# Kernel optimization log

Hardware: AMD Instinct MI355X
Metric: run time of the kernel (lower is better)

The kernel has to match this reference:

```python
import jax, jax.numpy as jnp
import numpy as np

N_NODES = 100000
N_EDGES = 1600000
IN_DIM = 75
H_COMP = 64
H_BOND = 16
DEPTH = 3


def setup_inputs() -> dict:
    key = jax.random.key(0)
    ks = jax.random.split(key, 8)
    x = jax.random.normal(ks[0], (N_NODES, IN_DIM), dtype=jnp.float32)
    edge_index = jax.random.randint(ks[1], (2, N_EDGES), 0, N_NODES, dtype=jnp.int64)
    edge_attr = jax.random.normal(ks[2], (N_EDGES, H_BOND), dtype=jnp.float32)
    proj_w = jax.random.normal(ks[3], (IN_DIM, H_COMP), dtype=jnp.float32) * (1.0 / np.sqrt(IN_DIM))
    proj_b = jnp.zeros((H_COMP,), dtype=jnp.float32)
    u2_w = jax.random.normal(ks[4], (DEPTH, H_COMP + H_BOND, H_COMP), dtype=jnp.float32) * (1.0 / np.sqrt(H_COMP + H_BOND))
    u2_b = jnp.zeros((DEPTH, H_COMP), dtype=jnp.float32)
    u1_w = jax.random.normal(ks[5], (DEPTH, 2 * H_COMP, H_COMP), dtype=jnp.float32) * (1.0 / np.sqrt(2 * H_COMP))
    u1_b = jnp.zeros((DEPTH, H_COMP), dtype=jnp.float32)
    return {"x": x, "edge_index": edge_index, "edge_attr": edge_attr,
            "proj_w": proj_w, "proj_b": proj_b,
            "u2_w": u2_w, "u2_b": u2_b, "u1_w": u1_w, "u1_b": u1_b}


def reference(x, edge_index, edge_attr, proj_w, proj_b, u2_w, u2_b, u1_w, u1_b):
    # PyG default flow source_to_target: messages gathered from edge_index[0],
    # scatter-added at edge_index[1].
    src, dst = edge_index[0], edge_index[1]
    n = x.shape[0]
    # input projection: [N, in_dim] -> [N, H]
    h = x @ proj_w + proj_b
    for l in range(u2_w.shape[0]):
        # message: concat(x_j, edge_attr) -> Linear -> LeakyReLU(0.1)   [E, H+B] -> [E, H]
        z = jnp.concatenate([h[src], edge_attr], axis=-1)
        m = jax.nn.leaky_relu(z @ u2_w[l] + u2_b[l], negative_slope=0.1)
        # aggregate: scatter-add over destination nodes  [E, H] -> [N, H]
        agg = jax.ops.segment_sum(m, dst, num_segments=n)
        # update: concat(x, agg) -> Linear  [N, 2H] -> [N, H]
        h = jnp.concatenate([h, agg], axis=-1) @ u1_w[l] + u1_b[l]
    return h
```

## Files before the change

### kernel.cpp

```cpp
#include <hip/hip_runtime.h>

typedef __attribute__((ext_vector_type(8))) short frag_ab;
typedef __attribute__((ext_vector_type(4))) float frag_cd;

__device__ __forceinline__ short f2bf(float f) {
  union { float f; unsigned u; } v; v.f = f;
  unsigned r = v.u + 0x7fffu + ((v.u >> 16) & 1u);
  return (short)(r >> 16);
}

__device__ __forceinline__ void wconv_body(
    const float* __restrict__ W, short* __restrict__ out,
    int Keff, int S, int nmat, int tid)
{
  int per = S * 4 * 64;
  if (tid >= nmat * per) return;
  int m = tid / per, r = tid % per;
  int s = r / 256, ct = (r >> 6) & 3, ln = r & 63;
  const float* Wm = W + (size_t)m * Keff * 64;
  __align__(16) short tmp[8];
  for (int j = 0; j < 8; ++j) {
    int k = s * 32 + (ln >> 4) * 8 + j;
    int n = ct * 16 + (ln & 15);
    tmp[j] = (k < Keff) ? f2bf(Wm[k * 64 + n]) : (short)0;
  }
  *(uint4*)&out[((size_t)m * per + (size_t)(s * 4 + ct) * 64 + ln) * 8] = *(uint4*)tmp;
}

__global__ void wconv_all(const float* __restrict__ pw,
                          const float* __restrict__ u2w,
                          const float* __restrict__ u1w,
                          short* projt, short* u2t, short* u1t)
{
  int b = blockIdx.x, t = threadIdx.x;
  if (b < 3)        wconv_body(pw,  projt, 75,  3, 1, b * 256 + t);
  else if (b < 12)  wconv_body(u2w, u2t,   80,  3, 3, (b - 3) * 256 + t);
  else              wconv_body(u1w, u1t,   128, 4, 3, (b - 12) * 256 + t);
}

#define AS1 104
__global__ __launch_bounds__(256, 4) void proj_kernel(
    const float* __restrict__ x, const short* __restrict__ wt,
    const float* __restrict__ bias, short* __restrict__ hbf, int N)
{
  __shared__ __align__(16) short A[128 * AS1];
  int t = threadIdx.x;
  int nb = blockIdx.x * 128;
  int ln = t & 63;
  frag_ab bf[12];
  for (int s = 0; s < 3; ++s)
    for (int ct = 0; ct < 4; ++ct)
      bf[s * 4 + ct] = *(const frag_ab*)&wt[((size_t)(s * 4 + ct) * 64 + ln) * 8];
  for (int i = 0; i < 48; ++i) {
    int q = i * 256 + t; int el = q / 96; int c = q - el * 96;
    int rg = nb + el;
    float v = (c < 75 && rg < N) ? x[rg * 75 + c] : 0.f;
    A[el * AS1 + c] = f2bf(v);
  }
  __syncthreads();
  int wv = t >> 6;
  int lrow = ln & 15, lk = ln >> 4;
  frag_cd acc[2][4];
  for (int rt = 0; rt < 2; ++rt) for (int ct = 0; ct < 4; ++ct) {
    frag_cd z = {0.f, 0.f, 0.f, 0.f}; acc[rt][ct] = z;
  }
  for (int s = 0; s < 3; ++s) {
    frag_ab a0 = *(const frag_ab*)&A[(wv*32 + lrow) * AS1 + s*32 + lk*8];
    frag_ab a1 = *(const frag_ab*)&A[(wv*32 + 16 + lrow) * AS1 + s*32 + lk*8];
    for (int ct = 0; ct < 4; ++ct) {
      acc[0][ct] = __builtin_amdgcn_mfma_f32_16x16x32_bf16(a0, bf[s*4+ct], acc[0][ct], 0, 0, 0);
      acc[1][ct] = __builtin_amdgcn_mfma_f32_16x16x32_bf16(a1, bf[s*4+ct], acc[1][ct], 0, 0, 0);
    }
  }
  float bv[4];
  for (int ct = 0; ct < 4; ++ct) bv[ct] = bias[ct*16 + lrow];
  for (int rt = 0; rt < 2; ++rt)
    for (int ct = 0; ct < 4; ++ct)
      for (int r = 0; r < 4; ++r) {
        int row = wv*32 + rt*16 + lk*4 + r;
        int rg = nb + row;
        if (rg < N) hbf[(size_t)rg * 64 + ct*16 + lrow] = f2bf(acc[rt][ct][r] + bv[ct]);
      }
}

__global__ __launch_bounds__(256) void hist_kernel(
    const int* __restrict__ dst, int* __restrict__ counts,
    int* __restrict__ rank, int E)
{
  int i = blockIdx.x * 256 + threadIdx.x;
  if (i < E) rank[i] = atomicAdd(&counts[dst[i]], 1);
}

#define SCAN_TILE 2048
__global__ __launch_bounds__(256) void scan_k1(
    const int* __restrict__ counts, int* __restrict__ offsets,
    int* __restrict__ bsum, int n)
{
  __shared__ int ts[256];
  int t = threadIdx.x;
  int base = blockIdx.x * SCAN_TILE + t * 8;
  int v[8]; int s = 0;
  for (int j = 0; j < 8; ++j) { v[j] = (base + j < n) ? counts[base + j] : 0; s += v[j]; }
  ts[t] = s; __syncthreads();
  for (int off = 1; off < 256; off <<= 1) {
    int x = (t >= off) ? ts[t - off] : 0;
    __syncthreads();
    ts[t] += x;
    __syncthreads();
  }
  if (t == 255) bsum[blockIdx.x] = ts[255];
  int run = (t > 0) ? ts[t - 1] : 0;
  for (int j = 0; j < 8; ++j) { if (base + j < n) offsets[base + j] = run; run += v[j]; }
}

__global__ __launch_bounds__(256) void scan_k3(
    int* __restrict__ offsets, const int* __restrict__ bsum, int n, int nb)
{
  __shared__ int adds;
  int t = threadIdx.x;
  if (t < 64) {
    int v = (t < nb) ? bsum[t] : 0;
    int x = v;
    for (int o = 1; o < 64; o <<= 1) { int y = __shfl_up(x, o); if (t >= o) x += y; }
    int b = blockIdx.x;
    int a = __shfl(x, b - 1);
    if (t == 0) adds = (b == 0) ? 0 : a;
  }
  __syncthreads();
  int add = adds;
  int base = blockIdx.x * SCAN_TILE + t;
  for (int j = 0; j < 8; ++j) { int i = base + j * 256; if (i < n) offsets[i] += add; }
}

__global__ __launch_bounds__(256) void scatter_kernel(
    const int* __restrict__ src, const int* __restrict__ dst,
    const float* __restrict__ attr, const int* __restrict__ offsets,
    const int* __restrict__ rank, uint4* __restrict__ rec, int E)
{
  int e = blockIdx.x * 256 + threadIdx.x;
  if (e < E) {
    int d = dst[e];
    int p = offsets[d] + rank[e];
    const float4* a4 = (const float4*)(attr + (size_t)e * 16);
    float4 v0 = a4[0], v1 = a4[1], v2 = a4[2], v3 = a4[3];
    __align__(16) short tmp[16];
    tmp[0]=f2bf(v0.x); tmp[1]=f2bf(v0.y); tmp[2]=f2bf(v0.z); tmp[3]=f2bf(v0.w);
    tmp[4]=f2bf(v1.x); tmp[5]=f2bf(v1.y); tmp[6]=f2bf(v1.z); tmp[7]=f2bf(v1.w);
    tmp[8]=f2bf(v2.x); tmp[9]=f2bf(v2.y); tmp[10]=f2bf(v2.z); tmp[11]=f2bf(v2.w);
    tmp[12]=f2bf(v3.x); tmp[13]=f2bf(v3.y); tmp[14]=f2bf(v3.z); tmp[15]=f2bf(v3.w);
    uint4* rp = rec + (size_t)p * 4;
    uint4 q0; q0.x = (unsigned)src[e]; q0.y = (unsigned)d; q0.z = 0u; q0.w = 0u;
    uint4 qz = {0u, 0u, 0u, 0u};
    rp[0] = q0;
    rp[1] = *(uint4*)&tmp[0];
    rp[2] = *(uint4*)&tmp[8];
    rp[3] = qz;
  }
}

#define MS 66
__global__ __launch_bounds__(256, 4) void msg_kernel(
    const short* __restrict__ hbf, const uint4* __restrict__ rec,
    const short* __restrict__ wt, const float* __restrict__ bias,
    float* __restrict__ agg, int E)
{
  __shared__ float M[128 * MS];
  __shared__ int dstl[128];
  int t = threadIdx.x;
  int eb = blockIdx.x * 128;
  int ln = t & 63;
  int wv = t >> 6;
  int lrow = ln & 15, lk = ln >> 4;

  if (t < 128) {
    int p = eb + t;
    dstl[t] = (p < E) ? ((const int*)(rec + (size_t)p * 4))[1] : -1;
  }

  int p0 = eb + wv*32 + lrow;  if (p0 > E - 1) p0 = E - 1;
  int p1 = p0 + 16;            if (p1 > E - 1) p1 = E - 1;
  int s0 = ((const int*)(rec + (size_t)p0 * 4))[0];
  int s1 = ((const int*)(rec + (size_t)p1 * 4))[0];

  frag_ab a[3][2];
  a[0][0] = *(const frag_ab*)&hbf[(size_t)s0 * 64 + lk*8];
  a[0][1] = *(const frag_ab*)&hbf[(size_t)s1 * 64 + lk*8];
  a[1][0] = *(const frag_ab*)&hbf[(size_t)s0 * 64 + 32 + lk*8];
  a[1][1] = *(const frag_ab*)&hbf[(size_t)s1 * 64 + 32 + lk*8];
  frag_ab z8 = {0,0,0,0,0,0,0,0};
  a[2][0] = (lk < 2) ? *(const frag_ab*)((const short*)(rec + (size_t)p0 * 4) + 8 + lk*8) : z8;
  a[2][1] = (lk < 2) ? *(const frag_ab*)((const short*)(rec + (size_t)p1 * 4) + 8 + lk*8) : z8;

  frag_cd acc[2][4];
  for (int rt = 0; rt < 2; ++rt) for (int ct = 0; ct < 4; ++ct) {
    frag_cd z = {0.f, 0.f, 0.f, 0.f}; acc[rt][ct] = z;
  }
  for (int s = 0; s < 3; ++s)
    for (int ct = 0; ct < 4; ++ct) {
      frag_ab b = *(const frag_ab*)&wt[((size_t)(s * 4 + ct) * 64 + ln) * 8];
      acc[0][ct] = __builtin_amdgcn_mfma_f32_16x16x32_bf16(a[s][0], b, acc[0][ct], 0, 0, 0);
      acc[1][ct] = __builtin_amdgcn_mfma_f32_16x16x32_bf16(a[s][1], b, acc[1][ct], 0, 0, 0);
    }
  float bv[4];
  for (int ct = 0; ct < 4; ++ct) bv[ct] = bias[ct*16 + lrow];

  for (int rt = 0; rt < 2; ++rt)
    for (int ct = 0; ct < 4; ++ct)
      for (int r = 0; r < 4; ++r) {
        int row = wv*32 + rt*16 + lk*4 + r;
        float m = acc[rt][ct][r] + bv[ct];
        m = m > 0.f ? m : 0.1f * m;
        M[row * MS + ct*16 + lrow] = m;
      }
  __syncthreads();

  {
    int lo = wv * 32;
    bool end = false;
    if (ln < 32) {
      int di = dstl[lo + ln];
      end = (ln == 31) || (di != dstl[lo + ln + 1]);
    }
    unsigned long long bm = __ballot(end);
    unsigned em = (unsigned)bm;
    unsigned cm = em & ~(em & (0u - em)) & 0x7fffffffu;

    float s = 0.f;
#pragma unroll
    for (int i = 0; i < 32; ++i) {
      s += M[(lo + i) * MS + ln];
      if ((em >> i) & 1u) {
        int d = __builtin_amdgcn_readfirstlane(dstl[lo + i]);
        if (d >= 0) {
          float* dest = &agg[(size_t)d * 64 + ln];
          if ((cm >> i) & 1u) *dest = s;
          else unsafeAtomicAdd(dest, s);
        }
        s = 0.f;
      }
    }
  }
}

__global__ __launch_bounds__(256, 4) void upd_kernel(
    const short* __restrict__ hbf, float* __restrict__ agg,
    const short* __restrict__ wt, const float* __restrict__ bias,
    float* __restrict__ hout, short* __restrict__ hbfo, int N, int last)
{
  int t = threadIdx.x;
  int nb = blockIdx.x * 128;
  int ln = t & 63;
  int wv = t >> 6;
  int lrow = ln & 15, lk = ln >> 4;
  int r0 = nb + wv*32 + lrow;
  int r1 = r0 + 16;

  frag_ab z8 = {0,0,0,0,0,0,0,0};
  frag_ab a[4][2];
  a[0][0] = (r0 < N) ? *(const frag_ab*)&hbf[(size_t)r0 * 64 + lk*8]      : z8;
  a[0][1] = (r1 < N) ? *(const frag_ab*)&hbf[(size_t)r1 * 64 + lk*8]      : z8;
  a[1][0] = (r0 < N) ? *(const frag_ab*)&hbf[(size_t)r0 * 64 + 32 + lk*8] : z8;
  a[1][1] = (r1 < N) ? *(const frag_ab*)&hbf[(size_t)r1 * 64 + 32 + lk*8] : z8;
  for (int si = 0; si < 2; ++si) {
    int cb = si * 32 + lk * 8;
    for (int rt = 0; rt < 2; ++rt) {
      int rg = rt ? r1 : r0;
      frag_ab af = z8;
      if (rg < N) {
        float* ap = &agg[(size_t)rg * 64 + cb];
        float4 v0 = *(const float4*)ap;
        float4 v1 = *(const float4*)(ap + 4);
        af[0]=f2bf(v0.x); af[1]=f2bf(v0.y); af[2]=f2bf(v0.z); af[3]=f2bf(v0.w);
        af[4]=f2bf(v1.x); af[5]=f2bf(v1.y); af[6]=f2bf(v1.z); af[7]=f2bf(v1.w);
        if (!last) {
          float4 z = make_float4(0.f, 0.f, 0.f, 0.f);
          *(float4*)ap = z; *(float4*)(ap + 4) = z;
        }
      }
      a[2 + si][rt] = af;
    }
  }

  frag_cd acc[2][4];
  for (int rt = 0; rt < 2; ++rt) for (int ct = 0; ct < 4; ++ct) {
    frag_cd z = {0.f, 0.f, 0.f, 0.f}; acc[rt][ct] = z;
  }
  for (int s = 0; s < 4; ++s)
    for (int ct = 0; ct < 4; ++ct) {
      frag_ab b = *(const frag_ab*)&wt[((size_t)(s * 4 + ct) * 64 + ln) * 8];
      acc[0][ct] = __builtin_amdgcn_mfma_f32_16x16x32_bf16(a[s][0], b, acc[0][ct], 0, 0, 0);
      acc[1][ct] = __builtin_amdgcn_mfma_f32_16x16x32_bf16(a[s][1], b, acc[1][ct], 0, 0, 0);
    }
  float bv[4];
  for (int ct = 0; ct < 4; ++ct) bv[ct] = bias[ct*16 + lrow];
  for (int rt = 0; rt < 2; ++rt)
    for (int ct = 0; ct < 4; ++ct)
      for (int r = 0; r < 4; ++r) {
        int row = wv*32 + rt*16 + lk*4 + r;
        int rg = nb + row;
        if (rg < N) {
          float v = acc[rt][ct][r] + bv[ct];
          if (last) hout[(size_t)rg * 64 + ct*16 + lrow] = v;
          hbfo[(size_t)rg * 64 + ct*16 + lrow] = f2bf(v);
        }
      }
}

extern "C" void kernel_launch(void* const* d_in, const int* in_sizes, int n_in,
                              void* d_out, int out_size, void* d_ws, size_t ws_size,
                              hipStream_t stream) {
  const float* x    = (const float*)d_in[0];
  const int*   ei   = (const int*)d_in[1];
  const float* attr = (const float*)d_in[2];
  const float* pw   = (const float*)d_in[3];
  const float* pb   = (const float*)d_in[4];
  const float* u2w  = (const float*)d_in[5];
  const float* u2b  = (const float*)d_in[6];
  const float* u1w  = (const float*)d_in[7];
  const float* u1b  = (const float*)d_in[8];

  const int N = in_sizes[0] / 75;
  const int E = in_sizes[1] / 2;
  const int* src = ei;
  const int* dst = ei + E;

  float* hout = (float*)d_out;
  char*  ws   = (char*)d_ws;
  size_t nh   = (size_t)N * 64;
  size_t off  = 0;
  short* hbf   = (short*)(ws + off); off += nh * 2;
  float* agg   = (float*)(ws + off); off += nh * 4;
  uint4* rec   = (uint4*)(ws + off); off += (size_t)E * 64;
  short* projt = (short*)(ws + off); off += 3 * 4 * 64 * 8 * 2;
  short* u2t   = (short*)(ws + off); off += (size_t)3 * 3 * 4 * 64 * 8 * 2;
  short* u1t   = (short*)(ws + off); off += (size_t)3 * 4 * 4 * 64 * 8 * 2;
  int* counts  = (int*)agg;
  int* offsets = counts + N;
  int* bsum    = offsets + N;
  int* rank    = bsum + 64;

  const int NB = (N + 127) / 128;
  const int EB = (E + 127) / 128;
  const int GE = (E + 255) / 256;
  const int NS = (N + SCAN_TILE - 1) / SCAN_TILE;

  wconv_all<<<24, 256, 0, stream>>>(pw, u2w, u1w, projt, u2t, u1t);
  proj_kernel<<<NB, 256, 0, stream>>>(x, projt, pb, hbf, N);
  hipMemsetAsync(counts, 0, (size_t)N * 4, stream);
  hist_kernel<<<GE, 256, 0, stream>>>(dst, counts, rank, E);
  scan_k1<<<NS, 256, 0, stream>>>(counts, offsets, bsum, N);
  scan_k3<<<NS, 256, 0, stream>>>(offsets, bsum, N, NS);
  scatter_kernel<<<GE, 256, 0, stream>>>(src, dst, attr, offsets, rank, rec, E);

  hipMemsetAsync(agg, 0, nh * 4, stream);
  for (int l = 0; l < 3; ++l) {
    msg_kernel<<<EB, 256, 0, stream>>>(hbf, rec,
                                       u2t + (size_t)l * 6144, u2b + l * 64,
                                       agg, E);
    upd_kernel<<<NB, 256, 0, stream>>>(hbf, agg,
                                       u1t + (size_t)l * 8192, u1b + l * 64,
                                       hout, hbf, N, l == 2);
  }
}
```

Baseline: 702.8 us.

## Make message aggregation wave-local with bf16 LDS staging and smaller update tiles

New measurement: 644.7 us. 8.3% less time.

```diff
diff --git a/kernel.cpp b/kernel.cpp
--- a/kernel.cpp
+++ b/kernel.cpp
@@ -7,6 +7,10 @@
   union { float f; unsigned u; } v; v.f = f;
   unsigned r = v.u + 0x7fffu + ((v.u >> 16) & 1u);
   return (short)(r >> 16);
+}
+__device__ __forceinline__ float bf2f(short s) {
+  union { unsigned u; float f; } v; v.u = ((unsigned)(unsigned short)s) << 16;
+  return v.f;
 }
 
 __device__ __forceinline__ void wconv_body(
@@ -159,34 +163,33 @@
 }
 
 #define MS 66
-__global__ __launch_bounds__(256, 4) void msg_kernel(
+__global__ __launch_bounds__(256, 6) void msg_kernel(
     const short* __restrict__ hbf, const uint4* __restrict__ rec,
     const short* __restrict__ wt, const float* __restrict__ bias,
     float* __restrict__ agg, int E)
 {
-  __shared__ float M[128 * MS];
-  __shared__ int dstl[128];
+  __shared__ short M2[128 * MS];
   int t = threadIdx.x;
   int eb = blockIdx.x * 128;
   int ln = t & 63;
   int wv = t >> 6;
   int lrow = ln & 15, lk = ln >> 4;
-
-  if (t < 128) {
-    int p = eb + t;
-    dstl[t] = (p < E) ? ((const int*)(rec + (size_t)p * 4))[1] : -1;
-  }
-
-  int p0 = eb + wv*32 + lrow;  if (p0 > E - 1) p0 = E - 1;
-  int p1 = p0 + 16;            if (p1 > E - 1) p1 = E - 1;
-  int s0 = ((const int*)(rec + (size_t)p0 * 4))[0];
-  int s1 = ((const int*)(rec + (size_t)p1 * 4))[0];
+  int lo = wv * 32;
+
+  int g0 = eb + lo + lrow;
+  int g1 = g0 + 16;
+  int p0 = g0 > E - 1 ? E - 1 : g0;
+  int p1 = g1 > E - 1 ? E - 1 : g1;
+  int2 sd0 = *(const int2*)(rec + (size_t)p0 * 4);
+  int2 sd1 = *(const int2*)(rec + (size_t)p1 * 4);
+  int d0 = (g0 < E) ? sd0.y : -1;
+  int d1 = (g1 < E) ? sd1.y : -1;
 
   frag_ab a[3][2];
-  a[0][0] = *(const frag_ab*)&hbf[(size_t)s0 * 64 + lk*8];
-  a[0][1] = *(const frag_ab*)&hbf[(size_t)s1 * 64 + lk*8];
-  a[1][0] = *(const frag_ab*)&hbf[(size_t)s0 * 64 + 32 + lk*8];
-  a[1][1] = *(const frag_ab*)&hbf[(size_t)s1 * 64 + 32 + lk*8];
+  a[0][0] = *(const frag_ab*)&hbf[(size_t)sd0.x * 64 + lk*8];
+  a[0][1] = *(const frag_ab*)&hbf[(size_t)sd1.x * 64 + lk*8];
+  a[1][0] = *(const frag_ab*)&hbf[(size_t)sd0.x * 64 + 32 + lk*8];
+  a[1][1] = *(const frag_ab*)&hbf[(size_t)sd1.x * 64 + 32 + lk*8];
   frag_ab z8 = {0,0,0,0,0,0,0,0};
   a[2][0] = (lk < 2) ? *(const frag_ab*)((const short*)(rec + (size_t)p0 * 4) + 8 + lk*8) : z8;
   a[2][1] = (lk < 2) ? *(const frag_ab*)((const short*)(rec + (size_t)p1 * 4) + 8 + lk*8) : z8;
@@ -207,37 +210,31 @@
   for (int rt = 0; rt < 2; ++rt)
     for (int ct = 0; ct < 4; ++ct)
       for (int r = 0; r < 4; ++r) {
-        int row = wv*32 + rt*16 + lk*4 + r;
+        int row = lo + rt*16 + lk*4 + r;
         float m = acc[rt][ct][r] + bv[ct];
         m = m > 0.f ? m : 0.1f * m;
-        M[row * MS + ct*16 + lrow] = m;
-      }
-  __syncthreads();
-
-  {
-    int lo = wv * 32;
-    bool end = false;
-    if (ln < 32) {
-      int di = dstl[lo + ln];
-      end = (ln == 31) || (di != dstl[lo + ln + 1]);
-    }
-    unsigned long long bm = __ballot(end);
-    unsigned em = (unsigned)bm;
-    unsigned cm = em & ~(em & (0u - em)) & 0x7fffffffu;
-
-    float s = 0.f;
+        M2[row * MS + ct*16 + lrow] = f2bf(m);
+      }
+  __asm__ __volatile__("s_waitcnt lgkmcnt(0)" ::: "memory");
+
+  int dl = (ln < 16) ? d0 : d1;
+  int dnext = __shfl_down(dl, 1);
+  bool end = (ln < 32) && ((ln == 31) || (dl != dnext));
+  unsigned em = (unsigned)__ballot(end);
+  unsigned cm = em & ~(em & (0u - em)) & 0x7fffffffu;
+
+  float s = 0.f;
 #pragma unroll
-    for (int i = 0; i < 32; ++i) {
-      s += M[(lo + i) * MS + ln];
-      if ((em >> i) & 1u) {
-        int d = __builtin_amdgcn_readfirstlane(dstl[lo + i]);
-        if (d >= 0) {
-          float* dest = &agg[(size_t)d * 64 + ln];
-          if ((cm >> i) & 1u) *dest = s;
-          else unsafeAtomicAdd(dest, s);
-        }
-        s = 0.f;
-      }
+  for (int i = 0; i < 32; ++i) {
+    s += bf2f(M2[(lo + i) * MS + ln]);
+    if ((em >> i) & 1u) {
+      int di = (i < 16) ? __shfl(d0, i) : __shfl(d1, i - 16);
+      if (di >= 0) {
+        float* dest = &agg[(size_t)di * 64 + ln];
+        if ((cm >> i) & 1u) *dest = s;
+        else unsafeAtomicAdd(dest, s);
+      }
+      s = 0.f;
     }
   }
 }
@@ -248,62 +245,53 @@
     float* __restrict__ hout, short* __restrict__ hbfo, int N, int last)
 {
   int t = threadIdx.x;
-  int nb = blockIdx.x * 128;
+  int nb = blockIdx.x * 64;
   int ln = t & 63;
   int wv = t >> 6;
   int lrow = ln & 15, lk = ln >> 4;
-  int r0 = nb + wv*32 + lrow;
-  int r1 = r0 + 16;
+  int r0 = nb + wv*16 + lrow;
 
   frag_ab z8 = {0,0,0,0,0,0,0,0};
-  frag_ab a[4][2];
-  a[0][0] = (r0 < N) ? *(const frag_ab*)&hbf[(size_t)r0 * 64 + lk*8]      : z8;
-  a[0][1] = (r1 < N) ? *(const frag_ab*)&hbf[(size_t)r1 * 64 + lk*8]      : z8;
-  a[1][0] = (r0 < N) ? *(const frag_ab*)&hbf[(size_t)r0 * 64 + 32 + lk*8] : z8;
-  a[1][1] = (r1 < N) ? *(const frag_ab*)&hbf[(size_t)r1 * 64 + 32 + lk*8] : z8;
+  frag_ab a[4];
+  a[0] = (r0 < N) ? *(const frag_ab*)&hbf[(size_t)r0 * 64 + lk*8]      : z8;
+  a[1] = (r0 < N) ? *(const frag_ab*)&hbf[(size_t)r0 * 64 + 32 + lk*8] : z8;
   for (int si = 0; si < 2; ++si) {
     int cb = si * 32 + lk * 8;
-    for (int rt = 0; rt < 2; ++rt) {
-      int rg = rt ? r1 : r0;
-      frag_ab af = z8;
-      if (rg < N) {
-        float* ap = &agg[(size_t)rg * 64 + cb];
-        float4 v0 = *(const float4*)ap;
-        float4 v1 = *(const float4*)(ap + 4);
-        af[0]=f2bf(v0.x); af[1]=f2bf(v0.y); af[2]=f2bf(v0.z); af[3]=f2bf(v0.w);
-        af[4]=f2bf(v1.x); af[5]=f2bf(v1.y); af[6]=f2bf(v1.z); af[7]=f2bf(v1.w);
-        if (!last) {
-          float4 z = make_float4(0.f, 0.f, 0.f, 0.f);
-          *(float4*)ap = z; *(float4*)(ap + 4) = z;
-        }
-      }
-      a[2 + si][rt] = af;
-    }
-  }
-
-  frag_cd acc[2][4];
-  for (int rt = 0; rt < 2; ++rt) for (int ct = 0; ct < 4; ++ct) {
-    frag_cd z = {0.f, 0.f, 0.f, 0.f}; acc[rt][ct] = z;
+    frag_ab af = z8;
+    if (r0 < N) {
+      float* ap = &agg[(size_t)r0 * 64 + cb];
+      float4 v0 = *(const float4*)ap;
+      float4 v1 = *(const float4*)(ap + 4);
+      af[0]=f2bf(v0.x); af[1]=f2bf(v0.y); af[2]=f2bf(v0.z); af[3]=f2bf(v0.w);
+      af[4]=f2bf(v1.x); af[5]=f2bf(v1.y); af[6]=f2bf(v1.z); af[7]=f2bf(v1.w);
+      if (!last) {
+        float4 z = make_float4(0.f, 0.f, 0.f, 0.f);
+        *(float4*)ap = z; *(float4*)(ap + 4) = z;
+      }
+    }
+    a[2 + si] = af;
+  }
+
+  frag_cd acc[4];
+  for (int ct = 0; ct < 4; ++ct) {
+    frag_cd z = {0.f, 0.f, 0.f, 0.f}; acc[ct] = z;
   }
   for (int s = 0; s < 4; ++s)
     for (int ct = 0; ct < 4; ++ct) {
       frag_ab b = *(const frag_ab*)&wt[((size_t)(s * 4 + ct) * 64 + ln) * 8];
-      acc[0][ct] = __builtin_amdgcn_mfma_f32_16x16x32_bf16(a[s][0], b, acc[0][ct], 0, 0, 0);
-      acc[1][ct] = __builtin_amdgcn_mfma_f32_16x16x32_bf16(a[s][1], b, acc[1][ct], 0, 0, 0);
+      acc[ct] = __builtin_amdgcn_mfma_f32_16x16x32_bf16(a[s], b, acc[ct], 0, 0, 0);
     }
   float bv[4];
   for (int ct = 0; ct < 4; ++ct) bv[ct] = bias[ct*16 + lrow];
-  for (int rt = 0; rt < 2; ++rt)
-    for (int ct = 0; ct < 4; ++ct)
-      for (int r = 0; r < 4; ++r) {
-        int row = wv*32 + rt*16 + lk*4 + r;
-        int rg = nb + row;
-        if (rg < N) {
-          float v = acc[rt][ct][r] + bv[ct];
-          if (last) hout[(size_t)rg * 64 + ct*16 + lrow] = v;
-          hbfo[(size_t)rg * 64 + ct*16 + lrow] = f2bf(v);
-        }
-      }
+  for (int ct = 0; ct < 4; ++ct)
+    for (int r = 0; r < 4; ++r) {
+      int rg = nb + wv*16 + lk*4 + r;
+      if (rg < N) {
+        float v = acc[ct][r] + bv[ct];
+        if (last) hout[(size_t)rg * 64 + ct*16 + lrow] = v;
+        hbfo[(size_t)rg * 64 + ct*16 + lrow] = f2bf(v);
+      }
+    }
 }
 
 extern "C" void kernel_launch(void* const* d_in, const int* in_sizes, int n_in,
@@ -340,6 +328,7 @@
   int* rank    = bsum + 64;
 
   const int NB = (N + 127) / 128;
+  const int NB2 = (N + 63) / 64;
   const int EB = (E + 127) / 128;
   const int GE = (E + 255) / 256;
   const int NS = (N + SCAN_TILE - 1) / SCAN_TILE;
@@ -357,8 +346,8 @@
     msg_kernel<<<EB, 256, 0, stream>>>(hbf, rec,
                                        u2t + (size_t)l * 6144, u2b + l * 64,
                                        agg, E);
-    upd_kernel<<<NB, 256, 0, stream>>>(hbf, agg,
-                                       u1t + (size_t)l * 8192, u1b + l * 64,
-                                       hout, hbf, N, l == 2);
-  }
-}
+    upd_kernel<<<NB2, 256, 0, stream>>>(hbf, agg,
+                                        u1t + (size_t)l * 8192, u1b + l * 64,
+                                        hout, hbf, N, l == 2);
+  }
+}
```
